# Performance work log

Hardware: AMD Instinct MI355X
Metric: run time of the kernel (lower is better)

## Reference

```python
import jax, jax.numpy as jnp
import numpy as np

EMBED = 1024
HEADS = 16
HEAD_SIZE = EMBED // HEADS
B, T = 2, 2048
EPS = 1e-5


def layer_norm(x, g, b):
    mu = jnp.mean(x, axis=-1, keepdims=True)
    var = jnp.var(x, axis=-1, keepdims=True)
    return (x - mu) * jax.lax.rsqrt(var + EPS) * g + b


def setup_inputs() -> dict:
    key = jax.random.key(0)
    ks = jax.random.split(key, 12)
    s = 0.02
    return {
        "x": jax.random.normal(ks[0], (B, T, EMBED), jnp.float32),
        "Wq": s * jax.random.normal(ks[1], (EMBED, EMBED), jnp.float32),
        "Wk": s * jax.random.normal(ks[2], (EMBED, EMBED), jnp.float32),
        "Wv": s * jax.random.normal(ks[3], (EMBED, EMBED), jnp.float32),
        "Wo": s * jax.random.normal(ks[4], (EMBED, EMBED), jnp.float32),
        "bo": jnp.zeros((EMBED,), jnp.float32),
        "W1": s * jax.random.normal(ks[5], (EMBED, 4 * EMBED), jnp.float32),
        "b1": jnp.zeros((4 * EMBED,), jnp.float32),
        "W2": s * jax.random.normal(ks[6], (4 * EMBED, EMBED), jnp.float32),
        "b2": jnp.zeros((EMBED,), jnp.float32),
        "ln1_g": jnp.ones((EMBED,), jnp.float32),
        "ln1_b": jnp.zeros((EMBED,), jnp.float32),
        "ln2_g": jnp.ones((EMBED,), jnp.float32),
        "ln2_b": jnp.zeros((EMBED,), jnp.float32),
    }


def reference(x, Wq, Wk, Wv, Wo, bo, W1, b1, W2, b2, ln1_g, ln1_b, ln2_g, ln2_b):
    # --- multi-head causal self-attention on ln1(x) ---
    h = layer_norm(x, ln1_g, ln1_b)                      # [B,T,D]
    q = (h @ Wq).reshape(B, T, HEADS, HEAD_SIZE)         # per-head Q (concat layout)
    k = (h @ Wk).reshape(B, T, HEADS, HEAD_SIZE)
    v = (h @ Wv).reshape(B, T, HEADS, HEAD_SIZE)
    scores = jnp.einsum("bqhd,bkhd->bhqk", q, k) / jnp.sqrt(
        jnp.asarray(HEAD_SIZE, x.dtype)
    )                                                    # [B,H,T,T]
    causal = jnp.tril(jnp.ones((T, T), bool))
    scores = jnp.where(causal, scores, -jnp.inf)
    wei = jax.nn.softmax(scores, axis=-1)
    attn = jnp.einsum("bhqk,bkhd->bqhd", wei, v).reshape(B, T, EMBED)
    x = x + attn @ Wo + bo                               # residual (dropout=0)
    # --- feed-forward on ln2(x) ---
    h2 = layer_norm(x, ln2_g, ln2_b)
    ff = jax.nn.relu(h2 @ W1 + b1) @ W2 + b2
    return x + ff
```

## Files before the change

### kernel.cpp

```cpp
#include <hip/hip_runtime.h>


typedef __bf16 bf16;
typedef __attribute__((ext_vector_type(8))) __bf16 bf16x8;
typedef __attribute__((ext_vector_type(4))) __bf16 bf16x4;
typedef __attribute__((ext_vector_type(4))) short  shortx4;
typedef __attribute__((ext_vector_type(4))) float  floatx4;

__device__ __forceinline__ short f2bf_bits(float x) {
  return __builtin_bit_cast(short, (bf16)x);
}

__device__ __forceinline__ void gl2lds16(const bf16* g, bf16* l) {
  __builtin_amdgcn_global_load_lds((const __attribute__((address_space(1))) void*)g,
                                   (__attribute__((address_space(3))) void*)l, 16, 0, 0);
}

__global__ __launch_bounds__(256) void prep_kernel(
    const float* __restrict__ Wq, const float* __restrict__ Wk,
    const float* __restrict__ Wv, const float* __restrict__ Wo,
    const float* __restrict__ W1, const float* __restrict__ W2,
    bf16* __restrict__ WqkvT, bf16* __restrict__ WoT,
    bf16* __restrict__ W1T, bf16* __restrict__ W2T,
    const float* __restrict__ x, const float* __restrict__ ln1g,
    const float* __restrict__ ln1b, bf16* __restrict__ h1)
{
  int id = blockIdx.x;
  if (id >= 12288) {
    const int row = id - 12288, t = threadIdx.x;
    const float* xr = x + (size_t)row * 1024;
    float4 v = *(const float4*)(xr + t * 4);
    float s  = v.x + v.y + v.z + v.w;
    float s2 = v.x * v.x + v.y * v.y + v.z * v.z + v.w * v.w;
    #pragma unroll
    for (int off = 1; off < 64; off <<= 1) {
      s  += __shfl_xor(s, off);
      s2 += __shfl_xor(s2, off);
    }
    __shared__ float ps[4], ps2[4];
    int wv = t >> 6;
    if ((t & 63) == 0) { ps[wv] = s; ps2[wv] = s2; }
    __syncthreads();
    s  = ps[0] + ps[1] + ps[2] + ps[3];
    s2 = ps2[0] + ps2[1] + ps2[2] + ps2[3];
    const float mu = s * (1.0f / 1024.0f);
    const float rstd = rsqrtf(s2 * (1.0f / 1024.0f) - mu * mu + 1e-5f);
    float4 gv = *(const float4*)(ln1g + t * 4);
    float4 bv = *(const float4*)(ln1b + t * 4);
    bf16x4 o;
    o[0] = (bf16)((v.x - mu) * rstd * gv.x + bv.x);
    o[1] = (bf16)((v.y - mu) * rstd * gv.y + bv.y);
    o[2] = (bf16)((v.z - mu) * rstd * gv.z + bv.z);
    o[3] = (bf16)((v.w - mu) * rstd * gv.w + bv.w);
    *(bf16x4*)(h1 + (size_t)row * 1024 + t * 4) = o;
    return;
  }
  const float* src; bf16* dst; int K, N, tile;
  if (id < 4096) {
    K = 1024; N = 1024; tile = id & 1023;
    int wsel = id >> 10;
    src = (wsel == 0) ? Wq : (wsel == 1) ? Wk : (wsel == 2) ? Wv : Wo;
    dst = (wsel < 3) ? (WqkvT + (size_t)wsel * 1024 * 1024) : WoT;
  } else if (id < 8192) {
    K = 1024; N = 4096; tile = id - 4096; src = W1; dst = W1T;
  } else {
    K = 4096; N = 1024; tile = id - 8192; src = W2; dst = W2T;
  }
  int ntn = N >> 5;
  int k0 = (tile / ntn) * 32, n0 = (tile % ntn) * 32;
  __shared__ float tl[32][33];
  int tr = threadIdx.x >> 3, tc = (threadIdx.x & 7) * 4;
  float4 v = *(const float4*)(src + (size_t)(k0 + tr) * N + n0 + tc);
  tl[tr][tc + 0] = v.x; tl[tr][tc + 1] = v.y; tl[tr][tc + 2] = v.z; tl[tr][tc + 3] = v.w;
  __syncthreads();
  bf16x4 o = { (bf16)tl[tc + 0][tr], (bf16)tl[tc + 1][tr],
               (bf16)tl[tc + 2][tr], (bf16)tl[tc + 3][tr] };
  *(bf16x4*)(dst + (size_t)(n0 + tr) * K + k0 + tc) = o;
}

__device__ __forceinline__ void gemm_core(
    const bf16* __restrict__ A, const bf16* __restrict__ Bt,
    int Ktot, int k0, int k1, bf16* As, bf16* Bs, floatx4 (&acc)[4][4])
{
  const int tid = threadIdx.x, lane = tid & 63, wv = tid >> 6;
  const int li = lane & 15, g = lane >> 4;
  const int wm = wv >> 1, wn = wv & 1;
  const int srow = wv * 16 + (lane >> 2);
  const int scol = (lane & 3) * 8;
  const bf16* aP = A  + (size_t)srow * Ktot + scol;
  const bf16* bP = Bt + (size_t)srow * Ktot + scol;
  bf16* AsW = As + wv * 512;
  bf16* BsW = Bs + wv * 512;
  for (int kt = k0; kt < k1; kt += 64) {
    gl2lds16(aP + kt,                          AsW);
    gl2lds16(aP + kt + (size_t)64 * Ktot,      AsW + 2048);
    gl2lds16(aP + kt + 32,                     AsW + 4096);
    gl2lds16(aP + kt + 32 + (size_t)64 * Ktot, AsW + 6144);
    gl2lds16(bP + kt,                          BsW);
    gl2lds16(bP + kt + (size_t)64 * Ktot,      BsW + 2048);
    gl2lds16(bP + kt + 32,                     BsW + 4096);
    gl2lds16(bP + kt + 32 + (size_t)64 * Ktot, BsW + 6144);
    __syncthreads();
    #pragma unroll
    for (int hh = 0; hh < 2; ++hh) {
      const bf16* Ap = As + hh * 4096;
      const bf16* Bp = Bs + hh * 4096;
      bf16x8 af[4], bfr[4];
      #pragma unroll
      for (int r = 0; r < 4; ++r)
        af[r] = *(const bf16x8*)(Ap + (wm * 64 + r * 16 + li) * 32 + g * 8);
      #pragma unroll
      for (int c = 0; c < 4; ++c)
        bfr[c] = *(const bf16x8*)(Bp + (wn * 64 + c * 16 + li) * 32 + g * 8);
      #pragma unroll
      for (int r = 0; r < 4; ++r)
        #pragma unroll
        for (int c = 0; c < 4; ++c)
          acc[r][c] = __builtin_amdgcn_mfma_f32_16x16x32_bf16(bfr[c], af[r], acc[r][c], 0, 0, 0);
    }
    __syncthreads();
  }
}

template<bool BIAS, bool RELU, bool RESID>
__global__ __launch_bounds__(256) void gemm_kernel(
    const bf16* __restrict__ A, const bf16* __restrict__ Bt,
    const float* __restrict__ bias, const float* __restrict__ resid,
    bf16* __restrict__ Cb, float* __restrict__ Cf,
    int M, int N, int K)
{
  __shared__ bf16 As[128 * 64];
  __shared__ bf16 Bs[128 * 64];
  const int lane = threadIdx.x & 63, wv = threadIdx.x >> 6;
  const int li = lane & 15, g = lane >> 4;
  const int m0 = blockIdx.x * 128, n0 = blockIdx.y * 128;
  const int wm = wv >> 1, wn = wv & 1;
  floatx4 acc[4][4] = {};
  gemm_core(A + (size_t)m0 * K, Bt + (size_t)n0 * K, K, 0, K, As, Bs, acc);
  #pragma unroll
  for (int r = 0; r < 4; ++r) {
    int rowC = m0 + wm * 64 + r * 16 + li;
    #pragma unroll
    for (int c = 0; c < 4; ++c) {
      int colC = n0 + wn * 64 + c * 16 + g * 4;
      float4 bv = BIAS ? *(const float4*)(bias + colC) : float4{0, 0, 0, 0};
      float v0 = acc[r][c][0] + bv.x, v1 = acc[r][c][1] + bv.y;
      float v2 = acc[r][c][2] + bv.z, v3 = acc[r][c][3] + bv.w;
      if (RELU) {
        v0 = fmaxf(v0, 0.f); v1 = fmaxf(v1, 0.f);
        v2 = fmaxf(v2, 0.f); v3 = fmaxf(v3, 0.f);
      }
      size_t idx = (size_t)rowC * N + colC;
      if (RESID) {
        float4 rv = *(const float4*)(resid + idx);
        float4 ov = { v0 + rv.x, v1 + rv.y, v2 + rv.z, v3 + rv.w };
        *(float4*)(Cf + idx) = ov;
      } else {
        bf16x4 ov = { (bf16)v0, (bf16)v1, (bf16)v2, (bf16)v3 };
        *(bf16x4*)(Cb + idx) = ov;
      }
    }
  }
}

__global__ __launch_bounds__(256) void gemm_qkv(
    const bf16* __restrict__ A, const bf16* __restrict__ Bt,
    bf16* __restrict__ qkv, bf16* __restrict__ VtG)
{
  const int K = 1024;
  __shared__ bf16 As[128 * 64];
  __shared__ bf16 Bs[128 * 64];
  const int lane = threadIdx.x & 63, wv = threadIdx.x >> 6;
  const int li = lane & 15, g = lane >> 4;
  const int m0 = blockIdx.x * 128, n0 = blockIdx.y * 128;
  const int wm = wv >> 1, wn = wv & 1;
  floatx4 acc[4][4] = {};
  gemm_core(A + (size_t)m0 * K, Bt + (size_t)n0 * K, K, 0, K, As, Bs, acc);
  if (n0 < 2048) {
    #pragma unroll
    for (int r = 0; r < 4; ++r) {
      int rowC = m0 + wm * 64 + r * 16 + li;
      #pragma unroll
      for (int c = 0; c < 4; ++c) {
        int colC = n0 + wn * 64 + c * 16 + g * 4;
        bf16x4 ov = { (bf16)acc[r][c][0], (bf16)acc[r][c][1],
                      (bf16)acc[r][c][2], (bf16)acc[r][c][3] };
        *(bf16x4*)(qkv + (size_t)rowC * 3072 + colC) = ov;
      }
    }
  } else {
    #pragma unroll
    for (int r = 0; r < 4; ++r) {
      int rowC = m0 + wm * 64 + r * 16 + li;
      int key = rowC & 2047, bq = rowC >> 11;
      #pragma unroll
      for (int c = 0; c < 4; ++c) {
        int vcol0 = n0 + wn * 64 + c * 16 + g * 4 - 2048;
        #pragma unroll
        for (int e = 0; e < 4; ++e) {
          int vcol = vcol0 + e;
          int hh = vcol >> 6, d = vcol & 63;
          VtG[((size_t)(bq * 16 + hh) * 64 + d) * 2048 + key] = (bf16)acc[r][c][e];
        }
      }
    }
  }
}

__global__ __launch_bounds__(256) void gemm_splitk(
    const bf16* __restrict__ A, const bf16* __restrict__ Bt,
    bf16* __restrict__ Cp, int M, int N, int Ktot, int Kc)
{
  __shared__ bf16 As[128 * 64];
  __shared__ bf16 Bs[128 * 64];
  const int lane = threadIdx.x & 63, wv = threadIdx.x >> 6;
  const int li = lane & 15, g = lane >> 4;
  const int m0 = blockIdx.x * 128, n0 = blockIdx.y * 128;
  const int z = blockIdx.z;
  const int wm = wv >> 1, wn = wv & 1;
  floatx4 acc[4][4] = {};
  gemm_core(A + (size_t)m0 * Ktot, Bt + (size_t)n0 * Ktot, Ktot,
            z * Kc, (z + 1) * Kc, As, Bs, acc);
  bf16* C = Cp + (size_t)z * M * N;
  #pragma unroll
  for (int r = 0; r < 4; ++r) {
    int rowC = m0 + wm * 64 + r * 16 + li;
    #pragma unroll
    for (int c = 0; c < 4; ++c) {
      int colC = n0 + wn * 64 + c * 16 + g * 4;
      bf16x4 ov = { (bf16)acc[r][c][0], (bf16)acc[r][c][1],
                    (bf16)acc[r][c][2], (bf16)acc[r][c][3] };
      *(bf16x4*)(C + (size_t)rowC * N + colC) = ov;
    }
  }
}

__global__ __launch_bounds__(256) void combine_wo_ln2(
    const bf16* __restrict__ P, const float* __restrict__ bo,
    const float* __restrict__ x, const float* __restrict__ gam,
    const float* __restrict__ bet, float* __restrict__ x2, bf16* __restrict__ h2)
{
  const int row = blockIdx.x, t = threadIdx.x;
  const size_t base = (size_t)row * 1024 + t * 4;
  float4 v = *(const float4*)(x + base);
  bf16x4 p0 = *(const bf16x4*)(P + base);
  bf16x4 p1 = *(const bf16x4*)(P + 4194304 + base);
  float4 bv = *(const float4*)(bo + t * 4);
  v.x += (float)p0[0] + (float)p1[0] + bv.x;
  v.y += (float)p0[1] + (float)p1[1] + bv.y;
  v.z += (float)p0[2] + (float)p1[2] + bv.z;
  v.w += (float)p0[3] + (float)p1[3] + bv.w;
  *(float4*)(x2 + base) = v;
  float s  = v.x + v.y + v.z + v.w;
  float s2 = v.x * v.x + v.y * v.y + v.z * v.z + v.w * v.w;
  #pragma unroll
  for (int off = 1; off < 64; off <<= 1) {
    s  += __shfl_xor(s, off);
    s2 += __shfl_xor(s2, off);
  }
  __shared__ float ps[4], ps2[4];
  int wv = t >> 6;
  if ((t & 63) == 0) { ps[wv] = s; ps2[wv] = s2; }
  __syncthreads();
  s  = ps[0] + ps[1] + ps[2] + ps[3];
  s2 = ps2[0] + ps2[1] + ps2[2] + ps2[3];
  const float mu = s * (1.0f / 1024.0f);
  const float rstd = rsqrtf(s2 * (1.0f / 1024.0f) - mu * mu + 1e-5f);
  float4 gv = *(const float4*)(gam + t * 4);
  float4 bb = *(const float4*)(bet + t * 4);
  bf16x4 o;
  o[0] = (bf16)((v.x - mu) * rstd * gv.x + bb.x);
  o[1] = (bf16)((v.y - mu) * rstd * gv.y + bb.y);
  o[2] = (bf16)((v.z - mu) * rstd * gv.z + bb.z);
  o[3] = (bf16)((v.w - mu) * rstd * gv.w + bb.w);
  *(bf16x4*)(h2 + base) = o;
}

__global__ __launch_bounds__(256) void combine_ffn2(
    const bf16* __restrict__ P, const float* __restrict__ b2,
    const float* __restrict__ x2, float* __restrict__ out)
{
  const size_t i = ((size_t)blockIdx.x * 256 + threadIdx.x) * 4;
  const int col = (int)(i & 1023);
  float4 acc = *(const float4*)(x2 + i);
  float4 bv = *(const float4*)(b2 + col);
  acc.x += bv.x; acc.y += bv.y; acc.z += bv.z; acc.w += bv.w;
  #pragma unroll
  for (int z = 0; z < 4; ++z) {
    bf16x4 p = *(const bf16x4*)(P + (size_t)z * 4194304 + i);
    acc.x += (float)p[0]; acc.y += (float)p[1];
    acc.z += (float)p[2]; acc.w += (float)p[3];
  }
  *(float4*)(out + i) = acc;
}

__global__ __launch_bounds__(256, 2) void attn_kernel(
    const bf16* __restrict__ qkv, const bf16* __restrict__ VtG,
    bf16* __restrict__ attnb)
{
  __shared__ bf16 Ks[64 * 72];
  __shared__ bf16 Vt[64 * 72];
  const int t = threadIdx.x, lane = t & 63, wv = t >> 6;
  const int li = lane & 15, g = lane >> 4;
  const int p = blockIdx.x & 15, h = (blockIdx.x >> 4) & 15, b = blockIdx.x >> 8;
  const int row0 = b << 11;
  const int tlo = p * 4 + wv, thi = 127 - tlo;
  const int q0l = tlo << 4, q0h = thi << 4;
  const size_t qkvbase = (size_t)row0 * 3072 + (size_t)h * 64;
  const bf16* vgbase = VtG + (size_t)(b * 16 + h) * 64 * 2048;

  const bf16* qpl = qkv + qkvbase + (size_t)(q0l + li) * 3072 + g * 8;
  const bf16* qph = qkv + qkvbase + (size_t)(q0h + li) * 3072 + g * 8;
  bf16x8 bl0 = *(const bf16x8*)(qpl), bl1 = *(const bf16x8*)(qpl + 32);
  bf16x8 bh0 = *(const bf16x8*)(qph), bh1 = *(const bf16x8*)(qph + 32);

  floatx4 ol[4] = {}, oh[4] = {};
  float ll = 0.f, lh = 0.f;
  const int cmax = 31 - p;

  auto proc = [&](const bf16x8& bq0, const bf16x8& bq1, float& l_i,
                  floatx4 (&o)[4], int qg, int k0, bool diag) {
    floatx4 sv[4];
    #pragma unroll
    for (int s = 0; s < 4; ++s) {
      const bf16* kr = Ks + (s * 16 + li) * 72 + g * 8;
      bf16x8 a0 = *(const bf16x8*)(kr);
      bf16x8 a1 = *(const bf16x8*)(kr + 32);
      floatx4 z = {0.f, 0.f, 0.f, 0.f};
      z = __builtin_amdgcn_mfma_f32_16x16x32_bf16(a0, bq0, z, 0, 0, 0);
      z = __builtin_amdgcn_mfma_f32_16x16x32_bf16(a1, bq1, z, 0, 0, 0);
      sv[s] = z;
    }
    float pv[4][4];
    float rs = 0.f;
    #pragma unroll
    for (int s = 0; s < 4; ++s)
      #pragma unroll
      for (int e = 0; e < 4; ++e) {
        float val = __expf(sv[s][e] * 0.125f - 4.0f);
        if (diag) {
          int kg = k0 + s * 16 + g * 4 + e;
          val = (kg <= qg) ? val : 0.0f;
        }
        pv[s][e] = val;
        rs += val;
      }
    rs += __shfl_xor(rs, 16);
    rs += __shfl_xor(rs, 32);
    l_i += rs;
    #pragma unroll
    for (int s = 0; s < 4; ++s) {
      shortx4 bp = { f2bf_bits(pv[s][0]), f2bf_bits(pv[s][1]),
                     f2bf_bits(pv[s][2]), f2bf_bits(pv[s][3]) };
      #pragma unroll
      for (int c = 0; c < 4; ++c) {
        shortx4 av = *(const shortx4*)(Vt + (c * 16 + li) * 72 + s * 16 + g * 4);
        o[c] = __builtin_amdgcn_mfma_f32_16x16x16bf16_1k(av, bp, o[c], 0, 0, 0);
      }
    }
  };

  for (int c = 0; c <= cmax; ++c) {
    {
      const size_t kb = qkvbase + (size_t)(c * 64) * 3072 + 1024;
      #pragma unroll
      for (int r = 0; r < 2; ++r) {
        int row = r * 32 + (t >> 3), dc = (t & 7) * 8;
        bf16x8 kvv = *(const bf16x8*)(qkv + kb + (size_t)row * 3072 + dc);
        *(bf16x8*)(Ks + row * 72 + dc) = kvv;
      }
      int d = t >> 2, kg = (t & 3) * 16;
      const bf16* vg = vgbase + (size_t)d * 2048 + c * 64 + kg;
      bf16x8 v0 = *(const bf16x8*)(vg);
      bf16x8 v1 = *(const bf16x8*)(vg + 8);
      *(bf16x8*)(Vt + d * 72 + kg)     = v0;
      *(bf16x8*)(Vt + d * 72 + kg + 8) = v1;
    }
    __syncthreads();
    proc(bh0, bh1, lh, oh, q0h + li, c * 64, c == cmax);
    if (c <= p) proc(bl0, bl1, ll, ol, q0l + li, c * 64, c == p);
    __syncthreads();
  }

  const float invh = 1.0f / lh, invl = 1.0f / ll;
  #pragma unroll
  for (int c = 0; c < 4; ++c) {
    bf16x4 ovh = { (bf16)(oh[c][0] * invh), (bf16)(oh[c][1] * invh),
                   (bf16)(oh[c][2] * invh), (bf16)(oh[c][3] * invh) };
    *(bf16x4*)(attnb + (size_t)(row0 + q0h + li) * 1024 + h * 64 + c * 16 + g * 4) = ovh;
    bf16x4 ovl = { (bf16)(ol[c][0] * invl), (bf16)(ol[c][1] * invl),
                   (bf16)(ol[c][2] * invl), (bf16)(ol[c][3] * invl) };
    *(bf16x4*)(attnb + (size_t)(row0 + q0l + li) * 1024 + h * 64 + c * 16 + g * 4) = ovl;
  }
}

extern "C" void kernel_launch(void* const* d_in, const int* in_sizes, int n_in,
                              void* d_out, int out_size, void* d_ws, size_t ws_size,
                              hipStream_t stream) {
  (void)in_sizes; (void)n_in; (void)out_size; (void)ws_size;
  const float* x    = (const float*)d_in[0];
  const float* Wq   = (const float*)d_in[1];
  const float* Wk   = (const float*)d_in[2];
  const float* Wv   = (const float*)d_in[3];
  const float* Wo   = (const float*)d_in[4];
  const float* bo   = (const float*)d_in[5];
  const float* W1   = (const float*)d_in[6];
  const float* b1   = (const float*)d_in[7];
  const float* W2   = (const float*)d_in[8];
  const float* b2   = (const float*)d_in[9];
  const float* ln1g = (const float*)d_in[10];
  const float* ln1b = (const float*)d_in[11];
  const float* ln2g = (const float*)d_in[12];
  const float* ln2b = (const float*)d_in[13];
  float* out = (float*)d_out;
  char* ws = (char*)d_ws;

  constexpr size_t OFF_WQKVT = 0;
  constexpr size_t OFF_WOT   = OFF_WQKVT + 3072ull * 1024 * 2;
  constexpr size_t OFF_W1T   = OFF_WOT   + 1024ull * 1024 * 2;
  constexpr size_t OFF_W2T   = OFF_W1T   + 4096ull * 1024 * 2;
  constexpr size_t OFF_H1    = OFF_W2T   + 1024ull * 4096 * 2;
  constexpr size_t OFF_QKV   = OFF_H1    + 4096ull * 1024 * 2;
  constexpr size_t OFF_ATT   = OFF_QKV   + 4096ull * 3072 * 2;
  constexpr size_t OFF_X2    = OFF_ATT   + 4096ull * 1024 * 2;
  constexpr size_t OFF_H2    = OFF_X2    + 4096ull * 1024 * 4;
  constexpr size_t OFF_F1    = OFF_H2    + 4096ull * 1024 * 2;
  constexpr size_t OFF_PART  = OFF_F1    + 4096ull * 4096 * 2;
  constexpr size_t OFF_VTG   = OFF_PART  + 4ull * 4096 * 1024 * 2;

  bf16*  WqkvT = (bf16*)(ws + OFF_WQKVT);
  bf16*  WoT   = (bf16*)(ws + OFF_WOT);
  bf16*  W1T   = (bf16*)(ws + OFF_W1T);
  bf16*  W2T   = (bf16*)(ws + OFF_W2T);
  bf16*  h1    = (bf16*)(ws + OFF_H1);
  bf16*  qkv   = (bf16*)(ws + OFF_QKV);
  bf16*  attnb = (bf16*)(ws + OFF_ATT);
  float* x2    = (float*)(ws + OFF_X2);
  bf16*  h2    = (bf16*)(ws + OFF_H2);
  bf16*  f1    = (bf16*)(ws + OFF_F1);
  bf16*  part  = (bf16*)(ws + OFF_PART);
  bf16*  vtg   = (bf16*)(ws + OFF_VTG);

  prep_kernel<<<16384, 256, 0, stream>>>(Wq, Wk, Wv, Wo, W1, W2,
                                         WqkvT, WoT, W1T, W2T, x, ln1g, ln1b, h1);
  gemm_qkv<<<dim3(32, 24), 256, 0, stream>>>(h1, WqkvT, qkv, vtg);
  attn_kernel<<<512, 256, 0, stream>>>(qkv, vtg, attnb);
  gemm_splitk<<<dim3(32, 8, 2), 256, 0, stream>>>(attnb, WoT, part, 4096, 1024, 1024, 512);
  combine_wo_ln2<<<4096, 256, 0, stream>>>(part, bo, x, ln2g, ln2b, x2, h2);
  gemm_kernel<true, true, false><<<dim3(32, 32), 256, 0, stream>>>(
      h2, W1T, b1, nullptr, f1, nullptr, 4096, 4096, 1024);
  gemm_splitk<<<dim3(32, 8, 4), 256, 0, stream>>>(f1, W2T, part, 4096, 1024, 4096, 1024);
  combine_ffn2<<<4096, 256, 0, stream>>>(part, b2, x2, out);
}
```

Measured before the change: 348.3 us.

## Double-buffer GEMM LDS tiles with K-step 32 to overlap loads and MFMA

The shared GEMM core now loads 32-wide K slices into two alternating LDS buffers. It issues the next slice's global-to-LDS copy before computing on the current one, with one barrier per step instead of two. The goal is to hide global load latency behind MFMA work. The cost is twice as many loop iterations and barriers per K. The global_load_lds copies are asynchronous, so a single __syncthreads may not guarantee the next buffer is complete before it is read.

```diff
diff --git a/kernel.cpp b/kernel.cpp
--- a/kernel.cpp
+++ b/kernel.cpp
@@ -91,34 +91,33 @@
   const bf16* bP = Bt + (size_t)srow * Ktot + scol;
   bf16* AsW = As + wv * 512;
   bf16* BsW = Bs + wv * 512;
-  for (int kt = k0; kt < k1; kt += 64) {
-    gl2lds16(aP + kt,                          AsW);
-    gl2lds16(aP + kt + (size_t)64 * Ktot,      AsW + 2048);
-    gl2lds16(aP + kt + 32,                     AsW + 4096);
-    gl2lds16(aP + kt + 32 + (size_t)64 * Ktot, AsW + 6144);
-    gl2lds16(bP + kt,                          BsW);
-    gl2lds16(bP + kt + (size_t)64 * Ktot,      BsW + 2048);
-    gl2lds16(bP + kt + 32,                     BsW + 4096);
-    gl2lds16(bP + kt + 32 + (size_t)64 * Ktot, BsW + 6144);
+  auto stage = [&](int kt, int d) {
+    gl2lds16(aP + kt,                     AsW + d * 4096);
+    gl2lds16(aP + kt + (size_t)64 * Ktot, AsW + d * 4096 + 2048);
+    gl2lds16(bP + kt,                     BsW + d * 4096);
+    gl2lds16(bP + kt + (size_t)64 * Ktot, BsW + d * 4096 + 2048);
+  };
+  stage(k0, 0);
+  __syncthreads();
+  int cur = 0;
+  for (int kt = k0; kt < k1; kt += 32) {
+    if (kt + 32 < k1) stage(kt + 32, cur ^ 1);
+    const bf16* Ap = As + cur * 4096;
+    const bf16* Bp = Bs + cur * 4096;
+    bf16x8 af[4], bfr[4];
+    #pragma unroll
+    for (int r = 0; r < 4; ++r)
+      af[r] = *(const bf16x8*)(Ap + (wm * 64 + r * 16 + li) * 32 + g * 8);
+    #pragma unroll
+    for (int c = 0; c < 4; ++c)
+      bfr[c] = *(const bf16x8*)(Bp + (wn * 64 + c * 16 + li) * 32 + g * 8);
+    #pragma unroll
+    for (int r = 0; r < 4; ++r)
+      #pragma unroll
+      for (int c = 0; c < 4; ++c)
+        acc[r][c] = __builtin_amdgcn_mfma_f32_16x16x32_bf16(bfr[c], af[r], acc[r][c], 0, 0, 0);
     __syncthreads();
-    #pragma unroll
-    for (int hh = 0; hh < 2; ++hh) {
-      const bf16* Ap = As + hh * 4096;
-      const bf16* Bp = Bs + hh * 4096;
-      bf16x8 af[4], bfr[4];
-      #pragma unroll
-      for (int r = 0; r < 4; ++r)
-        af[r] = *(const bf16x8*)(Ap + (wm * 64 + r * 16 + li) * 32 + g * 8);
-      #pragma unroll
-      for (int c = 0; c < 4; ++c)
-        bfr[c] = *(const bf16x8*)(Bp + (wn * 64 + c * 16 + li) * 32 + g * 8);
-      #pragma unroll
-      for (int r = 0; r < 4; ++r)
-        #pragma unroll
-        for (int c = 0; c < 4; ++c)
-          acc[r][c] = __builtin_amdgcn_mfma_f32_16x16x32_bf16(bfr[c], af[r], acc[r][c], 0, 0, 0);
-    }
-    __syncthreads();
+    cur ^= 1;
   }
 }
 
@@ -129,8 +128,8 @@
     bf16* __restrict__ Cb, float* __restrict__ Cf,
     int M, int N, int K)
 {
-  __shared__ bf16 As[128 * 64];
-  __shared__ bf16 Bs[128 * 64];
+  __shared__ bf16 As[8192];
+  __shared__ bf16 Bs[8192];
   const int lane = threadIdx.x & 63, wv = threadIdx.x >> 6;
   const int li = lane & 15, g = lane >> 4;
   const int m0 = blockIdx.x * 128, n0 = blockIdx.y * 128;
@@ -168,8 +167,8 @@
     bf16* __restrict__ qkv, bf16* __restrict__ VtG)
 {
   const int K = 1024;
-  __shared__ bf16 As[128 * 64];
-  __shared__ bf16 Bs[128 * 64];
+  __shared__ bf16 As[8192];
+  __shared__ bf16 Bs[8192];
   const int lane = threadIdx.x & 63, wv = threadIdx.x >> 6;
   const int li = lane & 15, g = lane >> 4;
   const int m0 = blockIdx.x * 128, n0 = blockIdx.y * 128;
@@ -211,8 +210,8 @@
     const bf16* __restrict__ A, const bf16* __restrict__ Bt,
     bf16* __restrict__ Cp, int M, int N, int Ktot, int Kc)
 {
-  __shared__ bf16 As[128 * 64];
-  __shared__ bf16 Bs[128 * 64];
+  __shared__ bf16 As[8192];
+  __shared__ bf16 Bs[8192];
   const int lane = threadIdx.x & 63, wv = threadIdx.x >> 6;
   const int li = lane & 15, g = lane >> 4;
   const int m0 = blockIdx.x * 128, n0 = blockIdx.y * 128;
```

Measured after the change: 367.9 us. 5.6% more time.

## Switch GEMM core to 32x32x16 MFMA with swizzled LDS layout

Applied to the files above, without the earlier changes.

Replaces the 16x16x32 bf16 MFMA tiling (4x4 accumulators per wave) with 32x32x16 MFMAs (2x2 floatx16 accumulators). This cuts LDS fragment loads per K-step. It also rotates the global-to-LDS column placement by row to avoid LDS bank conflicts on fragment reads. All GEMM epilogues are rewritten for the new accumulator-to-output mapping. The risk is indexing errors in the swizzle or epilogue mapping, and a different register-pressure profile.

```diff
diff --git a/kernel.cpp b/kernel.cpp
--- a/kernel.cpp
+++ b/kernel.cpp
@@ -2,10 +2,11 @@
 
 
 typedef __bf16 bf16;
-typedef __attribute__((ext_vector_type(8))) __bf16 bf16x8;
-typedef __attribute__((ext_vector_type(4))) __bf16 bf16x4;
-typedef __attribute__((ext_vector_type(4))) short  shortx4;
-typedef __attribute__((ext_vector_type(4))) float  floatx4;
+typedef __attribute__((ext_vector_type(8)))  __bf16 bf16x8;
+typedef __attribute__((ext_vector_type(4)))  __bf16 bf16x4;
+typedef __attribute__((ext_vector_type(4)))  short  shortx4;
+typedef __attribute__((ext_vector_type(4)))  float  floatx4;
+typedef __attribute__((ext_vector_type(16))) float  floatx16;
 
 __device__ __forceinline__ short f2bf_bits(float x) {
   return __builtin_bit_cast(short, (bf16)x);
@@ -80,17 +81,23 @@
 
 __device__ __forceinline__ void gemm_core(
     const bf16* __restrict__ A, const bf16* __restrict__ Bt,
-    int Ktot, int k0, int k1, bf16* As, bf16* Bs, floatx4 (&acc)[4][4])
+    int Ktot, int k0, int k1, bf16* As, bf16* Bs, floatx16 (&acc)[2][2])
 {
   const int tid = threadIdx.x, lane = tid & 63, wv = tid >> 6;
-  const int li = lane & 15, g = lane >> 4;
+  const int r = lane & 31, hi = lane >> 5;
   const int wm = wv >> 1, wn = wv & 1;
   const int srow = wv * 16 + (lane >> 2);
-  const int scol = (lane & 3) * 8;
+  const int scol = (((lane & 3) + (srow & 3)) & 3) * 8;
   const bf16* aP = A  + (size_t)srow * Ktot + scol;
   const bf16* bP = Bt + (size_t)srow * Ktot + scol;
   bf16* AsW = As + wv * 512;
   bf16* BsW = Bs + wv * 512;
+  const int cc0 = ((0 + hi * 8 - (r & 3) * 8) & 31);
+  const int cc1 = ((16 + hi * 8 - (r & 3) * 8) & 31);
+  const bf16* a0P = As + (wm * 64 + r) * 32;
+  const bf16* a1P = As + (wm * 64 + 32 + r) * 32;
+  const bf16* b0P = Bs + (wn * 64 + r) * 32;
+  const bf16* b1P = Bs + (wn * 64 + 32 + r) * 32;
   for (int kt = k0; kt < k1; kt += 64) {
     gl2lds16(aP + kt,                          AsW);
     gl2lds16(aP + kt + (size_t)64 * Ktot,      AsW + 2048);
@@ -102,21 +109,20 @@
     gl2lds16(bP + kt + 32 + (size_t)64 * Ktot, BsW + 6144);
     __syncthreads();
     #pragma unroll
-    for (int hh = 0; hh < 2; ++hh) {
-      const bf16* Ap = As + hh * 4096;
-      const bf16* Bp = Bs + hh * 4096;
-      bf16x8 af[4], bfr[4];
-      #pragma unroll
-      for (int r = 0; r < 4; ++r)
-        af[r] = *(const bf16x8*)(Ap + (wm * 64 + r * 16 + li) * 32 + g * 8);
-      #pragma unroll
-      for (int c = 0; c < 4; ++c)
-        bfr[c] = *(const bf16x8*)(Bp + (wn * 64 + c * 16 + li) * 32 + g * 8);
-      #pragma unroll
-      for (int r = 0; r < 4; ++r)
-        #pragma unroll
-        for (int c = 0; c < 4; ++c)
-          acc[r][c] = __builtin_amdgcn_mfma_f32_16x16x32_bf16(bfr[c], af[r], acc[r][c], 0, 0, 0);
+    for (int h = 0; h < 2; ++h) {
+      const int pb = h * 4096;
+      #pragma unroll
+      for (int kh = 0; kh < 2; ++kh) {
+        const int cc = kh ? cc1 : cc0;
+        bf16x8 a0 = *(const bf16x8*)(a0P + pb + cc);
+        bf16x8 a1 = *(const bf16x8*)(a1P + pb + cc);
+        bf16x8 b0 = *(const bf16x8*)(b0P + pb + cc);
+        bf16x8 b1 = *(const bf16x8*)(b1P + pb + cc);
+        acc[0][0] = __builtin_amdgcn_mfma_f32_32x32x16_bf16(b0, a0, acc[0][0], 0, 0, 0);
+        acc[0][1] = __builtin_amdgcn_mfma_f32_32x32x16_bf16(b1, a0, acc[0][1], 0, 0, 0);
+        acc[1][0] = __builtin_amdgcn_mfma_f32_32x32x16_bf16(b0, a1, acc[1][0], 0, 0, 0);
+        acc[1][1] = __builtin_amdgcn_mfma_f32_32x32x16_bf16(b1, a1, acc[1][1], 0, 0, 0);
+      }
     }
     __syncthreads();
   }
@@ -129,35 +135,41 @@
     bf16* __restrict__ Cb, float* __restrict__ Cf,
     int M, int N, int K)
 {
-  __shared__ bf16 As[128 * 64];
-  __shared__ bf16 Bs[128 * 64];
+  __shared__ bf16 As[8192];
+  __shared__ bf16 Bs[8192];
   const int lane = threadIdx.x & 63, wv = threadIdx.x >> 6;
-  const int li = lane & 15, g = lane >> 4;
+  const int r = lane & 31, hi = lane >> 5;
   const int m0 = blockIdx.x * 128, n0 = blockIdx.y * 128;
   const int wm = wv >> 1, wn = wv & 1;
-  floatx4 acc[4][4] = {};
+  floatx16 acc[2][2] = {};
   gemm_core(A + (size_t)m0 * K, Bt + (size_t)n0 * K, K, 0, K, As, Bs, acc);
   #pragma unroll
-  for (int r = 0; r < 4; ++r) {
-    int rowC = m0 + wm * 64 + r * 16 + li;
-    #pragma unroll
-    for (int c = 0; c < 4; ++c) {
-      int colC = n0 + wn * 64 + c * 16 + g * 4;
-      float4 bv = BIAS ? *(const float4*)(bias + colC) : float4{0, 0, 0, 0};
-      float v0 = acc[r][c][0] + bv.x, v1 = acc[r][c][1] + bv.y;
-      float v2 = acc[r][c][2] + bv.z, v3 = acc[r][c][3] + bv.w;
-      if (RELU) {
-        v0 = fmaxf(v0, 0.f); v1 = fmaxf(v1, 0.f);
-        v2 = fmaxf(v2, 0.f); v3 = fmaxf(v3, 0.f);
-      }
-      size_t idx = (size_t)rowC * N + colC;
-      if (RESID) {
-        float4 rv = *(const float4*)(resid + idx);
-        float4 ov = { v0 + rv.x, v1 + rv.y, v2 + rv.z, v3 + rv.w };
-        *(float4*)(Cf + idx) = ov;
-      } else {
-        bf16x4 ov = { (bf16)v0, (bf16)v1, (bf16)v2, (bf16)v3 };
-        *(bf16x4*)(Cb + idx) = ov;
+  for (int rb = 0; rb < 2; ++rb) {
+    int m = m0 + wm * 64 + rb * 32 + r;
+    #pragma unroll
+    for (int cb = 0; cb < 2; ++cb) {
+      int nb = n0 + wn * 64 + cb * 32 + hi * 4;
+      #pragma unroll
+      for (int rg = 0; rg < 4; ++rg) {
+        int n = nb + rg * 8;
+        float4 bv = BIAS ? *(const float4*)(bias + n) : float4{0, 0, 0, 0};
+        float v0 = acc[rb][cb][rg * 4 + 0] + bv.x;
+        float v1 = acc[rb][cb][rg * 4 + 1] + bv.y;
+        float v2 = acc[rb][cb][rg * 4 + 2] + bv.z;
+        float v3 = acc[rb][cb][rg * 4 + 3] + bv.w;
+        if (RELU) {
+          v0 = fmaxf(v0, 0.f); v1 = fmaxf(v1, 0.f);
+          v2 = fmaxf(v2, 0.f); v3 = fmaxf(v3, 0.f);
+        }
+        size_t idx = (size_t)m * N + n;
+        if (RESID) {
+          float4 rv = *(const float4*)(resid + idx);
+          float4 ov = { v0 + rv.x, v1 + rv.y, v2 + rv.z, v3 + rv.w };
+          *(float4*)(Cf + idx) = ov;
+        } else {
+          bf16x4 ov = { (bf16)v0, (bf16)v1, (bf16)v2, (bf16)v3 };
+          *(bf16x4*)(Cb + idx) = ov;
+        }
       }
     }
   }
@@ -168,39 +180,47 @@
     bf16* __restrict__ qkv, bf16* __restrict__ VtG)
 {
   const int K = 1024;
-  __shared__ bf16 As[128 * 64];
-  __shared__ bf16 Bs[128 * 64];
+  __shared__ bf16 As[8192];
+  __shared__ bf16 Bs[8192];
   const int lane = threadIdx.x & 63, wv = threadIdx.x >> 6;
-  const int li = lane & 15, g = lane >> 4;
+  const int r = lane & 31, hi = lane >> 5;
   const int m0 = blockIdx.x * 128, n0 = blockIdx.y * 128;
   const int wm = wv >> 1, wn = wv & 1;
-  floatx4 acc[4][4] = {};
+  floatx16 acc[2][2] = {};
   gemm_core(A + (size_t)m0 * K, Bt + (size_t)n0 * K, K, 0, K, As, Bs, acc);
   if (n0 < 2048) {
     #pragma unroll
-    for (int r = 0; r < 4; ++r) {
-      int rowC = m0 + wm * 64 + r * 16 + li;
-      #pragma unroll
-      for (int c = 0; c < 4; ++c) {
-        int colC = n0 + wn * 64 + c * 16 + g * 4;
-        bf16x4 ov = { (bf16)acc[r][c][0], (bf16)acc[r][c][1],
-                      (bf16)acc[r][c][2], (bf16)acc[r][c][3] };
-        *(bf16x4*)(qkv + (size_t)rowC * 3072 + colC) = ov;
+    for (int rb = 0; rb < 2; ++rb) {
+      int m = m0 + wm * 64 + rb * 32 + r;
+      #pragma unroll
+      for (int cb = 0; cb < 2; ++cb) {
+        int nb = n0 + wn * 64 + cb * 32 + hi * 4;
+        #pragma unroll
+        for (int rg = 0; rg < 4; ++rg) {
+          int n = nb + rg * 8;
+          bf16x4 ov = { (bf16)acc[rb][cb][rg * 4 + 0], (bf16)acc[rb][cb][rg * 4 + 1],
+                        (bf16)acc[rb][cb][rg * 4 + 2], (bf16)acc[rb][cb][rg * 4 + 3] };
+          *(bf16x4*)(qkv + (size_t)m * 3072 + n) = ov;
+        }
       }
     }
   } else {
     #pragma unroll
-    for (int r = 0; r < 4; ++r) {
-      int rowC = m0 + wm * 64 + r * 16 + li;
-      int key = rowC & 2047, bq = rowC >> 11;
-      #pragma unroll
-      for (int c = 0; c < 4; ++c) {
-        int vcol0 = n0 + wn * 64 + c * 16 + g * 4 - 2048;
+    for (int rb = 0; rb < 2; ++rb) {
+      int m = m0 + wm * 64 + rb * 32 + r;
+      int key = m & 2047, bq = m >> 11;
+      #pragma unroll
+      for (int cb = 0; cb < 2; ++cb) {
+        int nb = n0 + wn * 64 + cb * 32 + hi * 4 - 2048;
         #pragma unroll
-        for (int e = 0; e < 4; ++e) {
-          int vcol = vcol0 + e;
-          int hh = vcol >> 6, d = vcol & 63;
-          VtG[((size_t)(bq * 16 + hh) * 64 + d) * 2048 + key] = (bf16)acc[r][c][e];
+        for (int rg = 0; rg < 4; ++rg) {
+          #pragma unroll
+          for (int e = 0; e < 4; ++e) {
+            int vcol = nb + rg * 8 + e;
+            int hh = vcol >> 6, d = vcol & 63;
+            VtG[((size_t)(bq * 16 + hh) * 64 + d) * 2048 + key] =
+                (bf16)acc[rb][cb][rg * 4 + e];
+          }
         }
       }
     }
@@ -211,26 +231,30 @@
     const bf16* __restrict__ A, const bf16* __restrict__ Bt,
     bf16* __restrict__ Cp, int M, int N, int Ktot, int Kc)
 {
-  __shared__ bf16 As[128 * 64];
-  __shared__ bf16 Bs[128 * 64];
+  __shared__ bf16 As[8192];
+  __shared__ bf16 Bs[8192];
   const int lane = threadIdx.x & 63, wv = threadIdx.x >> 6;
-  const int li = lane & 15, g = lane >> 4;
+  const int r = lane & 31, hi = lane >> 5;
   const int m0 = blockIdx.x * 128, n0 = blockIdx.y * 128;
   const int z = blockIdx.z;
   const int wm = wv >> 1, wn = wv & 1;
-  floatx4 acc[4][4] = {};
+  floatx16 acc[2][2] = {};
   gemm_core(A + (size_t)m0 * Ktot, Bt + (size_t)n0 * Ktot, Ktot,
             z * Kc, (z + 1) * Kc, As, Bs, acc);
   bf16* C = Cp + (size_t)z * M * N;
   #pragma unroll
-  for (int r = 0; r < 4; ++r) {
-    int rowC = m0 + wm * 64 + r * 16 + li;
-    #pragma unroll
-    for (int c = 0; c < 4; ++c) {
-      int colC = n0 + wn * 64 + c * 16 + g * 4;
-      bf16x4 ov = { (bf16)acc[r][c][0], (bf16)acc[r][c][1],
-                    (bf16)acc[r][c][2], (bf16)acc[r][c][3] };
-      *(bf16x4*)(C + (size_t)rowC * N + colC) = ov;
+  for (int rb = 0; rb < 2; ++rb) {
+    int m = m0 + wm * 64 + rb * 32 + r;
+    #pragma unroll
+    for (int cb = 0; cb < 2; ++cb) {
+      int nb = n0 + wn * 64 + cb * 32 + hi * 4;
+      #pragma unroll
+      for (int rg = 0; rg < 4; ++rg) {
+        int n = nb + rg * 8;
+        bf16x4 ov = { (bf16)acc[rb][cb][rg * 4 + 0], (bf16)acc[rb][cb][rg * 4 + 1],
+                      (bf16)acc[rb][cb][rg * 4 + 2], (bf16)acc[rb][cb][rg * 4 + 3] };
+        *(bf16x4*)(C + (size_t)m * N + n) = ov;
+      }
     }
   }
 }
```

After: 369.1 us. +6.0%, slower.

## Double-buffer K/V tiles in attention kernel with register prefetch

Applied to the files above, without the earlier changes.

The attention kernel now prefetches the next K/V chunk from global memory into registers while computing on the current LDS buffer, then writes it into a second LDS buffer. This removes one barrier per iteration and hides global load latency behind the MFMA work. In exchange it doubles attention LDS use and adds live registers under a launch bound of two blocks per SM, which could raise register pressure. The GEMM shared-array size edits are cosmetic and leave the sizes unchanged.

```diff
diff --git a/kernel.cpp b/kernel.cpp
--- a/kernel.cpp
+++ b/kernel.cpp
@@ -129,8 +129,8 @@
     bf16* __restrict__ Cb, float* __restrict__ Cf,
     int M, int N, int K)
 {
-  __shared__ bf16 As[128 * 64];
-  __shared__ bf16 Bs[128 * 64];
+  __shared__ bf16 As[8192];
+  __shared__ bf16 Bs[8192];
   const int lane = threadIdx.x & 63, wv = threadIdx.x >> 6;
   const int li = lane & 15, g = lane >> 4;
   const int m0 = blockIdx.x * 128, n0 = blockIdx.y * 128;
@@ -168,8 +168,8 @@
     bf16* __restrict__ qkv, bf16* __restrict__ VtG)
 {
   const int K = 1024;
-  __shared__ bf16 As[128 * 64];
-  __shared__ bf16 Bs[128 * 64];
+  __shared__ bf16 As[8192];
+  __shared__ bf16 Bs[8192];
   const int lane = threadIdx.x & 63, wv = threadIdx.x >> 6;
   const int li = lane & 15, g = lane >> 4;
   const int m0 = blockIdx.x * 128, n0 = blockIdx.y * 128;
@@ -211,8 +211,8 @@
     const bf16* __restrict__ A, const bf16* __restrict__ Bt,
     bf16* __restrict__ Cp, int M, int N, int Ktot, int Kc)
 {
-  __shared__ bf16 As[128 * 64];
-  __shared__ bf16 Bs[128 * 64];
+  __shared__ bf16 As[8192];
+  __shared__ bf16 Bs[8192];
   const int lane = threadIdx.x & 63, wv = threadIdx.x >> 6;
   const int li = lane & 15, g = lane >> 4;
   const int m0 = blockIdx.x * 128, n0 = blockIdx.y * 128;
@@ -298,8 +298,8 @@
     const bf16* __restrict__ qkv, const bf16* __restrict__ VtG,
     bf16* __restrict__ attnb)
 {
-  __shared__ bf16 Ks[64 * 72];
-  __shared__ bf16 Vt[64 * 72];
+  __shared__ bf16 Ks[2][64 * 72];
+  __shared__ bf16 Vt[2][64 * 72];
   const int t = threadIdx.x, lane = t & 63, wv = t >> 6;
   const int li = lane & 15, g = lane >> 4;
   const int p = blockIdx.x & 15, h = (blockIdx.x >> 4) & 15, b = blockIdx.x >> 8;
@@ -318,12 +318,32 @@
   float ll = 0.f, lh = 0.f;
   const int cmax = 31 - p;
 
-  auto proc = [&](const bf16x8& bq0, const bf16x8& bq1, float& l_i,
+  const int krow0 = t >> 3, kdc = (t & 7) * 8;
+  const int vd = t >> 2, vkg = (t & 3) * 16;
+  bf16x8 kv0, kv1, vv0, vv1;
+
+  auto ld = [&](int c) {
+    const size_t kb = qkvbase + (size_t)(c * 64) * 3072 + 1024;
+    kv0 = *(const bf16x8*)(qkv + kb + (size_t)krow0 * 3072 + kdc);
+    kv1 = *(const bf16x8*)(qkv + kb + (size_t)(krow0 + 32) * 3072 + kdc);
+    const bf16* vg = vgbase + (size_t)vd * 2048 + c * 64 + vkg;
+    vv0 = *(const bf16x8*)(vg);
+    vv1 = *(const bf16x8*)(vg + 8);
+  };
+  auto wr = [&](int buf) {
+    *(bf16x8*)(Ks[buf] + krow0 * 72 + kdc)        = kv0;
+    *(bf16x8*)(Ks[buf] + (krow0 + 32) * 72 + kdc) = kv1;
+    *(bf16x8*)(Vt[buf] + vd * 72 + vkg)           = vv0;
+    *(bf16x8*)(Vt[buf] + vd * 72 + vkg + 8)       = vv1;
+  };
+
+  auto proc = [&](const bf16* KsB, const bf16* VtB,
+                  const bf16x8& bq0, const bf16x8& bq1, float& l_i,
                   floatx4 (&o)[4], int qg, int k0, bool diag) {
     floatx4 sv[4];
     #pragma unroll
     for (int s = 0; s < 4; ++s) {
-      const bf16* kr = Ks + (s * 16 + li) * 72 + g * 8;
+      const bf16* kr = KsB + (s * 16 + li) * 72 + g * 8;
       bf16x8 a0 = *(const bf16x8*)(kr);
       bf16x8 a1 = *(const bf16x8*)(kr + 32);
       floatx4 z = {0.f, 0.f, 0.f, 0.f};
@@ -354,32 +374,23 @@
                      f2bf_bits(pv[s][2]), f2bf_bits(pv[s][3]) };
       #pragma unroll
       for (int c = 0; c < 4; ++c) {
-        shortx4 av = *(const shortx4*)(Vt + (c * 16 + li) * 72 + s * 16 + g * 4);
+        shortx4 av = *(const shortx4*)(VtB + (c * 16 + li) * 72 + s * 16 + g * 4);
         o[c] = __builtin_amdgcn_mfma_f32_16x16x16bf16_1k(av, bp, o[c], 0, 0, 0);
       }
     }
   };
 
+  ld(0);
+  wr(0);
+  __syncthreads();
+  int buf = 0;
   for (int c = 0; c <= cmax; ++c) {
-    {
-      const size_t kb = qkvbase + (size_t)(c * 64) * 3072 + 1024;
-      #pragma unroll
-      for (int r = 0; r < 2; ++r) {
-        int row = r * 32 + (t >> 3), dc = (t & 7) * 8;
-        bf16x8 kvv = *(const bf16x8*)(qkv + kb + (size_t)row * 3072 + dc);
-        *(bf16x8*)(Ks + row * 72 + dc) = kvv;
-      }
-      int d = t >> 2, kg = (t & 3) * 16;
-      const bf16* vg = vgbase + (size_t)d * 2048 + c * 64 + kg;
-      bf16x8 v0 = *(const bf16x8*)(vg);
-      bf16x8 v1 = *(const bf16x8*)(vg + 8);
-      *(bf16x8*)(Vt + d * 72 + kg)     = v0;
-      *(bf16x8*)(Vt + d * 72 + kg + 8) = v1;
-    }
+    if (c < cmax) ld(c + 1);
+    proc(Ks[buf], Vt[buf], bh0, bh1, lh, oh, q0h + li, c * 64, c == cmax);
+    if (c <= p) proc(Ks[buf], Vt[buf], bl0, bl1, ll, ol, q0l + li, c * 64, c == p);
+    if (c < cmax) wr(buf ^ 1);
     __syncthreads();
-    proc(bh0, bh1, lh, oh, q0h + li, c * 64, c == cmax);
-    if (c <= p) proc(bl0, bl1, ll, ol, q0l + li, c * 64, c == p);
-    __syncthreads();
+    buf ^= 1;
   }
 
   const float invh = 1.0f / lh, invl = 1.0f / ll;
```

Result: no change. 347.8 us (-0.1%).
